# Optimization experiments

Hardware: AMD Instinct MI355X
Metric: run time of the kernel (lower is better)

## Reference

```python
import jax, jax.numpy as jnp
import numpy as np

B, L, H, NH = 4, 200, 256, 4
HS = H // NH
NEG = jnp.float32(-(2.0**32) + 1.0)


def setup_inputs() -> dict:
    key = jax.random.key(0)
    ks = jax.random.split(key, 12)
    f = lambda k, s, sc=1.0: jax.random.normal(k, s, dtype=jnp.float32) * sc
    w_sc = 1.0 / np.sqrt(H).astype(np.float32)
    return {
        "queries": f(ks[0], (B, L, H)),
        "keys": f(ks[1], (B, L, H)),
        "time_matrix_K": f(ks[2], (B, L, L, H)),
        "time_matrix_V": f(ks[3], (B, L, L, H)),
        "dis_matrix_K": f(ks[4], (B, L, L, H)),
        "dis_matrix_V": f(ks[5], (B, L, L, H)),
        "abs_pos_K": f(ks[6], (B, L, H)),
        "abs_pos_V": f(ks[7], (B, L, H)),
        "Qw": f(ks[8], (H, H), w_sc),
        "Qb": jnp.zeros((H,), jnp.float32),
        "Kw": f(ks[9], (H, H), w_sc),
        "Kb": jnp.zeros((H,), jnp.float32),
        "Vw": f(ks[10], (H, H), w_sc),
        "Vb": jnp.zeros((H,), jnp.float32),
        "time_mask": jnp.zeros((B, L), dtype=bool),          # no padding positions
        "attn_mask": ~jnp.tril(jnp.ones((L, L), dtype=bool)),  # causal: mask strict upper triangle
    }


def reference(queries, keys, time_matrix_K, time_matrix_V, dis_matrix_K, dis_matrix_V,
              abs_pos_K, abs_pos_V, Qw, Qb, Kw, Kb, Vw, Vb, time_mask, attn_mask):
    # Linear projections (torch nn.Linear: x @ W^T + b)
    Q = queries @ Qw.T + Qb
    K = keys @ Kw.T + Kb
    V = keys @ Vw.T + Vb
    # split heads: [B, L, NH, HS]
    qh = Q.reshape(B, L, NH, HS)
    kh = K.reshape(B, L, NH, HS)
    vh = V.reshape(B, L, NH, HS)
    pKh = abs_pos_K.reshape(B, L, NH, HS)
    pVh = abs_pos_V.reshape(B, L, NH, HS)
    tKh = time_matrix_K.reshape(B, L, L, NH, HS)
    tVh = time_matrix_V.reshape(B, L, L, NH, HS)
    dKh = dis_matrix_K.reshape(B, L, L, NH, HS)
    dVh = dis_matrix_V.reshape(B, L, L, NH, HS)

    # attention logits [B, NH, L(query), L(key)] with three extra bias terms
    w = jnp.einsum("blhd,bmhd->bhlm", qh, kh)
    w += jnp.einsum("blhd,bmhd->bhlm", qh, pKh)
    w += jnp.einsum("blmhd,blhd->bhlm", tKh, qh)
    w += jnp.einsum("blmhd,blhd->bhlm", dKh, qh)
    w = w / jnp.sqrt(jnp.float32(HS))

    mask = time_mask[:, None, :, None] | attn_mask[None, None, :, :]
    w = jnp.where(mask, NEG, w)
    a = jax.nn.softmax(w, axis=-1)  # dropout_rate = 0 (eval)

    out = jnp.einsum("bhlm,bmhd->blhd", a, vh)
    out += jnp.einsum("bhlm,bmhd->blhd", a, pVh)
    out += jnp.einsum("bhlm,blmhd->blhd", a, tVh)
    out += jnp.einsum("bhlm,blmhd->blhd", a, dVh)
    return out.reshape(B, L, H)
```

## Files before the change

kernel.cpp:

```cpp
#include <hip/hip_runtime.h>
#include <cstddef>


#define B 4
#define L 200
#define H 256
#define NH 4
#define HS 64
#define SCALE 0.125f
#define NROWS 4

__global__ __launch_bounds__(256) void depoi_proj(
    const float* __restrict__ queries, const float* __restrict__ keys,
    const float* __restrict__ Qw, const float* __restrict__ Qb,
    const float* __restrict__ Kw, const float* __restrict__ Kb,
    const float* __restrict__ Vw, const float* __restrict__ Vb,
    const float* __restrict__ apK, const float* __restrict__ apV,
    float* __restrict__ Qo, float* __restrict__ Ko, float* __restrict__ Vo)
{
    __shared__ float4 xq[NROWS][H / 4];
    __shared__ float4 xk[NROWS][H / 4];
    const int t  = threadIdx.x;
    const int n0 = blockIdx.x * NROWS;

    const float4* q4 = (const float4*)queries;
    const float4* k4 = (const float4*)keys;
    {
        int r = t >> 6, c = t & 63;
        xq[r][c] = q4[(size_t)(n0 + r) * (H / 4) + c];
        xk[r][c] = k4[(size_t)(n0 + r) * (H / 4) + c];
    }
    __syncthreads();

    float accq[NROWS], acck[NROWS], accv[NROWS];
#pragma unroll
    for (int r = 0; r < NROWS; ++r) { accq[r] = 0.f; acck[r] = 0.f; accv[r] = 0.f; }

    const float4* Qw4 = (const float4*)Qw + (size_t)t * (H / 4);
    const float4* Kw4 = (const float4*)Kw + (size_t)t * (H / 4);
    const float4* Vw4 = (const float4*)Vw + (size_t)t * (H / 4);
    for (int i = 0; i < H / 4; ++i) {
        float4 wq = Qw4[i], wk = Kw4[i], wv = Vw4[i];
#pragma unroll
        for (int r = 0; r < NROWS; ++r) {
            float4 a = xq[r][i];
            float4 c = xk[r][i];
            accq[r] += a.x * wq.x + a.y * wq.y + a.z * wq.z + a.w * wq.w;
            acck[r] += c.x * wk.x + c.y * wk.y + c.z * wk.z + c.w * wk.w;
            accv[r] += c.x * wv.x + c.y * wv.y + c.z * wv.z + c.w * wv.w;
        }
    }

    const float bq = Qb[t], bk = Kb[t], bv = Vb[t];
#pragma unroll
    for (int r = 0; r < NROWS; ++r) {
        size_t o = (size_t)(n0 + r) * H + t;
        Qo[o] = accq[r] + bq;
        Ko[o] = acck[r] + bk + apK[o];
        Vo[o] = accv[r] + bv + apV[o];
    }
}

__global__ __launch_bounds__(512, 4) void depoi_attn(
    const float* __restrict__ Q, const float* __restrict__ Ksum,
    const float* __restrict__ Vsum,
    const float* __restrict__ tK, const float* __restrict__ dK,
    const float* __restrict__ tV, const float* __restrict__ dV,
    float* __restrict__ out)
{
    const int l  = L - 1 - blockIdx.x;
    const int b  = blockIdx.y;
    const int t  = threadIdx.x;
    const int c  = t & 63;
    const int mg = t >> 6;
    const int M  = l + 1;

    __shared__ float4 wacc[8][64];
    __shared__ float  wmax[8][NH];
    __shared__ float  wsum[8][NH];

    float4 q4 = ((const float4*)Q)[(size_t)(b * L + l) * 64 + c];
    q4.x *= SCALE; q4.y *= SCALE; q4.z *= SCALE; q4.w *= SCALE;

    const float4* K4  = (const float4*)Ksum + (size_t)b * L * 64 + c;
    const float4* V4  = (const float4*)Vsum + (size_t)b * L * 64 + c;
    const float4* T4  = (const float4*)tK + (size_t)(b * L + l) * L * 64 + c;
    const float4* D4  = (const float4*)dK + (size_t)(b * L + l) * L * 64 + c;
    const float4* TV4 = (const float4*)tV + (size_t)(b * L + l) * L * 64 + c;
    const float4* DV4 = (const float4*)dV + (size_t)(b * L + l) * L * 64 + c;

    float4 acc   = make_float4(0.f, 0.f, 0.f, 0.f);
    float  run_m = -3.0e38f;
    float  run_s = 0.f;

    int m = mg;
    for (; m + 8 < M; m += 16) {
        const size_t o0 = (size_t)m * 64;
        const size_t o1 = o0 + 512;
        float4 k0  = K4[o0],  k1  = K4[o1];
        float4 t0  = T4[o0],  t1  = T4[o1];
        float4 d0  = D4[o0],  d1  = D4[o1];
        float4 v0  = V4[o0],  v1  = V4[o1];
        float4 tv0 = TV4[o0], tv1 = TV4[o1];
        float4 dv0 = DV4[o0], dv1 = DV4[o1];
        __builtin_amdgcn_sched_barrier(0);

        float p0 = q4.x * (k0.x + t0.x + d0.x) + q4.y * (k0.y + t0.y + d0.y)
                 + q4.z * (k0.z + t0.z + d0.z) + q4.w * (k0.w + t0.w + d0.w);
        float p1 = q4.x * (k1.x + t1.x + d1.x) + q4.y * (k1.y + t1.y + d1.y)
                 + q4.z * (k1.z + t1.z + d1.z) + q4.w * (k1.w + t1.w + d1.w);
        p0 += __shfl_xor(p0, 1); p1 += __shfl_xor(p1, 1);
        p0 += __shfl_xor(p0, 2); p1 += __shfl_xor(p1, 2);
        p0 += __shfl_xor(p0, 4); p1 += __shfl_xor(p1, 4);
        p0 += __shfl_xor(p0, 8); p1 += __shfl_xor(p1, 8);

        float nm = fmaxf(run_m, fmaxf(p0, p1));
        float sc = __expf(run_m - nm);
        float e0 = __expf(p0 - nm);
        float e1 = __expf(p1 - nm);
        run_m = nm;
        run_s = run_s * sc + e0 + e1;
        acc.x = acc.x * sc + e0 * (v0.x + tv0.x + dv0.x) + e1 * (v1.x + tv1.x + dv1.x);
        acc.y = acc.y * sc + e0 * (v0.y + tv0.y + dv0.y) + e1 * (v1.y + tv1.y + dv1.y);
        acc.z = acc.z * sc + e0 * (v0.z + tv0.z + dv0.z) + e1 * (v1.z + tv1.z + dv1.z);
        acc.w = acc.w * sc + e0 * (v0.w + tv0.w + dv0.w) + e1 * (v1.w + tv1.w + dv1.w);
    }
    if (m < M) {
        const size_t o0 = (size_t)m * 64;
        float4 k0  = K4[o0];
        float4 t0  = T4[o0];
        float4 d0  = D4[o0];
        float4 v0  = V4[o0];
        float4 tv0 = TV4[o0];
        float4 dv0 = DV4[o0];
        __builtin_amdgcn_sched_barrier(0);
        float p0 = q4.x * (k0.x + t0.x + d0.x) + q4.y * (k0.y + t0.y + d0.y)
                 + q4.z * (k0.z + t0.z + d0.z) + q4.w * (k0.w + t0.w + d0.w);
        p0 += __shfl_xor(p0, 1);
        p0 += __shfl_xor(p0, 2);
        p0 += __shfl_xor(p0, 4);
        p0 += __shfl_xor(p0, 8);
        float nm = fmaxf(run_m, p0);
        float sc = __expf(run_m - nm);
        float e0 = __expf(p0 - nm);
        run_m = nm;
        run_s = run_s * sc + e0;
        acc.x = acc.x * sc + e0 * (v0.x + tv0.x + dv0.x);
        acc.y = acc.y * sc + e0 * (v0.y + tv0.y + dv0.y);
        acc.z = acc.z * sc + e0 * (v0.z + tv0.z + dv0.z);
        acc.w = acc.w * sc + e0 * (v0.w + tv0.w + dv0.w);
    }

    wacc[mg][c] = acc;
    if ((c & 15) == 0) {
        wmax[mg][c >> 4] = run_m;
        wsum[mg][c >> 4] = run_s;
    }
    __syncthreads();

    if (t < 64) {
        const int h = t >> 4;
        float gm = wmax[0][h];
#pragma unroll
        for (int i = 1; i < 8; ++i) gm = fmaxf(gm, wmax[i][h]);
        float4 r = make_float4(0.f, 0.f, 0.f, 0.f);
        float  s = 0.f;
#pragma unroll
        for (int i = 0; i < 8; ++i) {
            float sc = __expf(wmax[i][h] - gm);
            float4 w = wacc[i][t];
            r.x += sc * w.x; r.y += sc * w.y; r.z += sc * w.z; r.w += sc * w.w;
            s += sc * wsum[i][h];
        }
        const float inv = 1.0f / s;
        r.x *= inv; r.y *= inv; r.z *= inv; r.w *= inv;
        ((float4*)out)[(size_t)(b * L + l) * 64 + t] = r;
    }
}

extern "C" void kernel_launch(void* const* d_in, const int* in_sizes, int n_in,
                              void* d_out, int out_size, void* d_ws, size_t ws_size,
                              hipStream_t stream) {
    const float* queries = (const float*)d_in[0];
    const float* keys    = (const float*)d_in[1];
    const float* tK      = (const float*)d_in[2];
    const float* tV      = (const float*)d_in[3];
    const float* dK      = (const float*)d_in[4];
    const float* dV      = (const float*)d_in[5];
    const float* apK     = (const float*)d_in[6];
    const float* apV     = (const float*)d_in[7];
    const float* Qw      = (const float*)d_in[8];
    const float* Qb      = (const float*)d_in[9];
    const float* Kw      = (const float*)d_in[10];
    const float* Kb      = (const float*)d_in[11];
    const float* Vw      = (const float*)d_in[12];
    const float* Vb      = (const float*)d_in[13];

    float* ws = (float*)d_ws;
    float* Qo = ws;
    float* Ko = ws + (size_t)B * L * H;
    float* Vo = ws + (size_t)2 * B * L * H;

    depoi_proj<<<(B * L) / NROWS, 256, 0, stream>>>(
        queries, keys, Qw, Qb, Kw, Kb, Vw, Vb, apK, apV, Qo, Ko, Vo);

    dim3 grid(L, B);
    depoi_attn<<<grid, 512, 0, stream>>>(Qo, Ko, Vo, tK, dK, tV, dV, (float*)d_out);
}
```

Before: 538.8 us.

## Split attention key range into chunks across blocks with separate combine kernel

Each query row's key range is divided into 64-key chunks handled by separate 256-thread blocks, which write partial softmax states (accumulator, max, sum) to workspace. A new combine kernel merges the partials with log-sum-exp rescaling and normalizes. This aims to improve load balance and memory-level parallelism for the causal triangle, where row lengths vary widely. It costs an extra kernel launch and a workspace round trip for partial results.

Result: slower. 558.0 us (+3.6%).

```diff
diff --git a/kernel.cpp b/kernel.cpp
--- a/kernel.cpp
+++ b/kernel.cpp
@@ -9,6 +9,9 @@
 #define HS 64
 #define SCALE 0.125f
 #define NROWS 4
+#define CH 64
+#define NCMAX 4
+#define RECF 272
 
 __global__ __launch_bounds__(256) void depoi_proj(
     const float* __restrict__ queries, const float* __restrict__ keys,
@@ -61,23 +64,29 @@
     }
 }
 
-__global__ __launch_bounds__(512, 4) void depoi_attn(
+__global__ __launch_bounds__(256, 6) void depoi_attn(
     const float* __restrict__ Q, const float* __restrict__ Ksum,
     const float* __restrict__ Vsum,
     const float* __restrict__ tK, const float* __restrict__ dK,
     const float* __restrict__ tV, const float* __restrict__ dV,
-    float* __restrict__ out)
+    float* __restrict__ P)
 {
-    const int l  = L - 1 - blockIdx.x;
+    const int xc = blockIdx.x;
+    const int l  = L - 1 - (xc >> 2);
+    const int ci = xc & 3;
     const int b  = blockIdx.y;
+    const int M  = l + 1;
+    const int base = ci * CH;
+    if (base >= M) return;
+    const int lim = min(base + CH, M);
+
     const int t  = threadIdx.x;
     const int c  = t & 63;
     const int mg = t >> 6;
-    const int M  = l + 1;
-
-    __shared__ float4 wacc[8][64];
-    __shared__ float  wmax[8][NH];
-    __shared__ float  wsum[8][NH];
+
+    __shared__ float4 wacc[4][64];
+    __shared__ float  wmax[4][NH];
+    __shared__ float  wsum[4][NH];
 
     float4 q4 = ((const float4*)Q)[(size_t)(b * L + l) * 64 + c];
     q4.x *= SCALE; q4.y *= SCALE; q4.z *= SCALE; q4.w *= SCALE;
@@ -93,10 +102,10 @@
     float  run_m = -3.0e38f;
     float  run_s = 0.f;
 
-    int m = mg;
-    for (; m + 8 < M; m += 16) {
+    int m = base + mg;
+    for (; m + 4 < lim; m += 8) {
         const size_t o0 = (size_t)m * 64;
-        const size_t o1 = o0 + 512;
+        const size_t o1 = o0 + 256;
         float4 k0  = K4[o0],  k1  = K4[o1];
         float4 t0  = T4[o0],  t1  = T4[o1];
         float4 d0  = D4[o0],  d1  = D4[o1];
@@ -125,7 +134,7 @@
         acc.z = acc.z * sc + e0 * (v0.z + tv0.z + dv0.z) + e1 * (v1.z + tv1.z + dv1.z);
         acc.w = acc.w * sc + e0 * (v0.w + tv0.w + dv0.w) + e1 * (v1.w + tv1.w + dv1.w);
     }
-    if (m < M) {
+    if (m < lim) {
         const size_t o0 = (size_t)m * 64;
         float4 k0  = K4[o0];
         float4 t0  = T4[o0];
@@ -162,20 +171,53 @@
         const int h = t >> 4;
         float gm = wmax[0][h];
 #pragma unroll
-        for (int i = 1; i < 8; ++i) gm = fmaxf(gm, wmax[i][h]);
+        for (int i = 1; i < 4; ++i) gm = fmaxf(gm, wmax[i][h]);
         float4 r = make_float4(0.f, 0.f, 0.f, 0.f);
         float  s = 0.f;
 #pragma unroll
-        for (int i = 0; i < 8; ++i) {
+        for (int i = 0; i < 4; ++i) {
             float sc = __expf(wmax[i][h] - gm);
             float4 w = wacc[i][t];
             r.x += sc * w.x; r.y += sc * w.y; r.z += sc * w.z; r.w += sc * w.w;
             s += sc * wsum[i][h];
         }
-        const float inv = 1.0f / s;
-        r.x *= inv; r.y *= inv; r.z *= inv; r.w *= inv;
-        ((float4*)out)[(size_t)(b * L + l) * 64 + t] = r;
-    }
+        float* rec = P + (size_t)(((b * L + l) * NCMAX) + ci) * RECF;
+        ((float4*)rec)[t] = r;
+        if ((t & 15) == 0) {
+            rec[256 + h] = gm;
+            rec[260 + h] = s;
+        }
+    }
+}
+
+__global__ __launch_bounds__(256) void depoi_combine(
+    const float* __restrict__ P, float* __restrict__ out)
+{
+    const int t  = threadIdx.x;
+    const int p  = blockIdx.x * 4 + (t >> 6);
+    const int b  = p / L;
+    const int l  = p % L;
+    const int c  = t & 63;
+    const int h  = c >> 4;
+    const int nc = (l >> 6) + 1;
+
+    const float* rec0 = P + (size_t)((b * L + l) * NCMAX) * RECF;
+
+    float gm = -3.0e38f;
+    for (int ci = 0; ci < nc; ++ci) gm = fmaxf(gm, rec0[(size_t)ci * RECF + 256 + h]);
+
+    float4 r = make_float4(0.f, 0.f, 0.f, 0.f);
+    float  s = 0.f;
+    for (int ci = 0; ci < nc; ++ci) {
+        const float* rec = rec0 + (size_t)ci * RECF;
+        float sc = __expf(rec[256 + h] - gm);
+        float4 w = ((const float4*)rec)[c];
+        r.x += sc * w.x; r.y += sc * w.y; r.z += sc * w.z; r.w += sc * w.w;
+        s += sc * rec[260 + h];
+    }
+    const float inv = 1.0f / s;
+    r.x *= inv; r.y *= inv; r.z *= inv; r.w *= inv;
+    ((float4*)out)[(size_t)(b * L + l) * 64 + c] = r;
 }
 
 extern "C" void kernel_launch(void* const* d_in, const int* in_sizes, int n_in,
@@ -200,10 +242,13 @@
     float* Qo = ws;
     float* Ko = ws + (size_t)B * L * H;
     float* Vo = ws + (size_t)2 * B * L * H;
+    float* P  = ws + (size_t)3 * B * L * H;
 
     depoi_proj<<<(B * L) / NROWS, 256, 0, stream>>>(
         queries, keys, Qw, Qb, Kw, Kb, Vw, Vb, apK, apV, Qo, Ko, Vo);
 
-    dim3 grid(L, B);
-    depoi_attn<<<grid, 512, 0, stream>>>(Qo, Ko, Vo, tK, dK, tV, dV, (float*)d_out);
-}
+    dim3 ga(L * NCMAX, B);
+    depoi_attn<<<ga, 256, 0, stream>>>(Qo, Ko, Vo, tK, dK, tV, dV, P);
+
+    depoi_combine<<<(B * L) / 4, 256, 0, stream>>>(P, (float*)d_out);
+}
```
